# Optimization experiments

Hardware: AMD Instinct MI355X
Metric: run time of the kernel (lower is better)

## Reference

```python
import jax, jax.numpy as jnp
import numpy as np

# Dimensions
NT, NS = 1000, 2048   # timesteps, basins
NF, NG = 6, 32        # forcing channels, static attributes
NH, NR, HS = 16, 8, 256  # buckets, routing taps, hidden size
NK, NGD = 3, 9        # len(kDict)=3 (km,ki,ke), len(gDict)=9


def setup_inputs() -> dict:
    key = jax.random.key(0)
    ks = jax.random.split(key, 16)
    # Physically plausible forcings: Prcp/Evp nonnegative, T1<=T2 (min/max temp)
    Prcp = jax.random.uniform(ks[0], (NT, NS)) * 10.0
    Evp = jax.random.uniform(ks[1], (NT, NS)) * 5.0
    Tm = jax.random.normal(ks[2], (NT, NS)) * 10.0
    T1 = Tm - jax.random.uniform(ks[3], (NT, NS)) * 5.0
    T2 = Tm + jax.random.uniform(ks[4], (NT, NS)) * 5.0
    Rad = jax.random.uniform(ks[5], (NT, NS))
    Hum = jax.random.uniform(ks[6], (NT, NS))
    x = jnp.stack([Prcp, Evp, T1, T2, Rad, Hum], axis=-1)  # [nt, ns, 6]
    xc = jax.random.normal(ks[7], (NS, NG))

    def lin(k, fan_in, fan_out, s=0.05):
        k1, k2 = jax.random.split(k)
        return (jax.random.normal(k1, (fan_in, fan_out)) * s,
                jax.random.normal(k2, (fan_out,)) * s)

    W_fc, b_fc = lin(ks[8], NG, HS)
    W_r, b_r = lin(ks[9], HS, NH * (NR + 1))
    W_g, b_g = lin(ks[10], HS, NH * NGD)
    W_kin, b_kin = lin(ks[11], 4, HS)
    W_kout, b_kout = lin(ks[12], HS, NH * NK)
    return dict(x=x, xc=xc, W_fc=W_fc, b_fc=b_fc, W_r=W_r, b_r=b_r,
                W_g=W_g, b_g=b_g, W_kin=W_kin, b_kin=b_kin,
                W_kout=W_kout, b_kout=b_kout)


def _hardsigmoid(v):
    return jnp.clip(v / 6.0 + 0.5, 0.0, 1.0)


def _forward(x, xc, W_fc, b_fc, W_r, b_r, W_g, b_g, W_kin, b_kin, W_kout, b_kout):
    nt, ns, _ = x.shape
    Prcp, Evp, T1, T2 = x[..., 0], x[..., 1], x[..., 2], x[..., 3]
    f = x[..., 2:]                        # [nt, ns, 4] (T1,T2,Rad,Hum)

    # ---- getParam (eval mode: DropMask is identity) ----
    state = xc @ W_fc + b_fc              # [ns, hs]
    pK = jnp.tanh(f @ W_kin + b_kin + state) @ W_kout + b_kout  # [nt, ns, nh*3]
    hG = jnp.tanh(state)
    pG = hG @ W_g + b_g                   # [ns, nh*9]
    pR = hG @ W_r + b_r                   # [ns, nh*(nr+1)]

    # sepParam(K): km=exp, ki=relu, ke=exp  -> time-varying [nt, ns, nh]
    km = jnp.exp(pK[..., 0 * NH:1 * NH])
    ki = jax.nn.relu(pK[..., 1 * NH:2 * NH])
    ke = jnp.exp(pK[..., 2 * NH:3 * NH])

    # sepParam(G): static [ns, nh]
    g = lambda i: pG[..., i * NH:(i + 1) * NH]
    kp = jax.nn.sigmoid(g(0))
    ks_ = jax.nn.sigmoid(g(1))
    kd = jax.nn.sigmoid(g(2))
    gd = jax.nn.sigmoid(g(3))
    gl = (jax.nn.sigmoid(g(4)) * 10.0) ** 3
    qb = jax.nn.relu(g(5)) / 10.0
    ga = jax.nn.softmax(g(6), axis=-1)    # area weights over buckets
    gi = _hardsigmoid(g(7)) / 2.0
    ge = jax.nn.relu(g(8))

    # onePeakWeight: unimodal routing weights [ns, nh, nr]
    r = pR.reshape(ns, NH, NR + 1)
    s = jax.nn.softmax(r, axis=-1)
    c = jnp.cumsum(s, axis=-1)
    w = jnp.minimum(c, 1.0 - c + s)[..., :NR]
    wr = w / jnp.sum(w, axis=-1, keepdims=True)

    # divideP: snow/liquid split from min/max temperature crossing 0 C
    fl = jnp.clip(T2 / (T2 - T1 + 1e-5), 0.0, 1.0)  # liquid fraction
    Pl = (Prcp * fl)[..., None]           # [nt, ns, 1]
    Ps = (Prcp * (1.0 - fl))[..., None]
    Ev = Evp[..., None]

    # ---- bucket.step recurrence over time (the custom-scan hot loop) ----
    def step(carry, inp):
        Sf, Ss, Sg = carry                # each [ns, nh]
        Ps_t, Pl_t, Ev_t, km_t, ki_t, ke_t = inp
        # snow bucket: accumulate, melt capped by degree-day factor km
        Sf = Sf + Ps_t
        qf = jnp.minimum(Sf, km_t)
        Sf = Sf - qf
        # partition inflow: impervious/direct fraction gi
        inflow = qf + Pl_t
        qd = inflow * gi
        Ss = Ss + inflow * (1.0 - gi)
        # evapotranspiration
        E = jnp.minimum(jnp.maximum(Ss, 0.0), Ev_t * ke_t * ge)
        Ss = Ss - E
        # interflow capped by ki
        qi = jnp.minimum(ki_t, jnp.maximum(Ss, 0.0))
        Ss = Ss - qi
        # quick flow above capacity gl, slow drainage below
        qp = kp * jnp.maximum(Ss - gl, 0.0)
        qsa = ks_ * jnp.clip(Ss, 0.0, gl)
        Ss = Ss - qp - qsa
        # deep/groundwater bucket: fraction gd percolates, linear reservoir kd + baseflow qb
        Sg = Sg + qsa * gd
        qg = kd * Sg + qb
        Sg = Sg * (1.0 - kd)
        q = qp + qsa * (1.0 - gd) + qg + qd + qi
        return (Sf, Ss, Sg), q

    init = (jnp.zeros((ns, NH), x.dtype),
            jnp.zeros((ns, NH), x.dtype),
            jnp.zeros((ns, NH), x.dtype))
    _, Qp = jax.lax.scan(step, init, (Ps, Pl, Ev, km, ki, ke))  # [nt, ns, nh]

    # routing: valid temporal convolution with per-bucket unit hydrograph wr
    Tout = nt - NR + 1
    Q = jnp.zeros((Tout, ns, NH), Qp.dtype)
    for rr in range(NR):  # NR is a small fixed constant
        Q = Q + Qp[NR - 1 - rr: nt - rr] * wr[..., rr]
    yOut = jnp.sum(Q * ga, axis=-1)       # [Tout, ns]
    return yOut


def reference(x, xc, W_fc, b_fc, W_r, b_r, W_g, b_g, W_kin, b_kin, W_kout, b_kout):
    return _forward(x, xc, W_fc, b_fc, W_r, b_r, W_g, b_g, W_kin, b_kin, W_kout, b_kout)
```

## Files before the change

### kernel.cpp

```cpp
#include <hip/hip_runtime.h>
#include <hip/hip_bf16.h>

#define NT   1000
#define NS   2048
#define NH   16
#define NR   8
#define HS   256
#define TOUT 993

typedef __attribute__((ext_vector_type(8))) short short8;
typedef __attribute__((ext_vector_type(4))) float f32x4;

__device__ __forceinline__ ushort f2bf(float f) {
    union { float f; unsigned int u; } v; v.f = f;
    unsigned int u = v.u;
    return (ushort)((u + 0x7fffu + ((u >> 16) & 1u)) >> 16);
}
__device__ __forceinline__ float bf2f(ushort u) {
    union { unsigned int i; float f; } v; v.i = ((unsigned int)u) << 16; return v.f;
}
__device__ __forceinline__ unsigned int packbf2(float lo, float hi) {
    union { __hip_bfloat162 b; unsigned int u; } v;
    v.b = __float22bfloat162_rn(make_float2(lo, hi));
    return v.u;
}
__device__ __forceinline__ float sigf(float x) { return 1.f / (1.f + __expf(-x)); }
__device__ __forceinline__ float fast_tanh(float z) {
    float e = exp2f(z * 2.885390082f);
    return 1.f - 2.f * __builtin_amdgcn_rcpf(e + 1.f);
}
template<int CTRL>
__device__ __forceinline__ float dpp_add(float v) {
    int s = __builtin_amdgcn_update_dpp(0, __builtin_bit_cast(int, v), CTRL, 0xf, 0xf, true);
    return v + __builtin_bit_cast(float, s);
}
__device__ __forceinline__ void gll16(const void* g, void* l) {
    __builtin_amdgcn_global_load_lds((const __attribute__((address_space(1))) unsigned int*)g,
                                     (__attribute__((address_space(3))) unsigned int*)l, 16, 0, 0);
}
__device__ __forceinline__ void gll4(const void* g, void* l) {
    __builtin_amdgcn_global_load_lds((const __attribute__((address_space(1))) unsigned int*)g,
                                     (__attribute__((address_space(3))) unsigned int*)l, 4, 0, 0);
}


__global__ __launch_bounds__(256) void kAw(
    const float* __restrict__ W_g, const float* __restrict__ W_r,
    const float* __restrict__ W_kin, const float* __restrict__ W_kout,
    ushort* __restrict__ WAhi, ushort* __restrict__ WAlo,
    ushort* __restrict__ Wt_g, ushort* __restrict__ whlo_g)
{
    const int tid = threadIdx.x, b = blockIdx.x;
    const int idx = b * 256 + tid;
    const int j = idx & 7, lane = (idx >> 3) & 63, chunk = idx >> 9;
    const int kc = chunk & 7, ct = chunk >> 3;
    const int col = ct * 16 + (lane & 15);
    const int k = kc * 32 + (lane >> 4) * 8 + j;
    const float* W = (col < 144) ? W_g : W_r;
    const int c2 = (col < 144) ? col : col - 144;
    const float w = W[k * 144 + c2];
    const ushort hi = f2bf(w);
    WAhi[idx] = hi;
    WAlo[idx] = f2bf(w - bf2f(hi));

    if (b == 0) {
        for (int i = tid; i < 48 * 256; i += 256) {
            int c = i % 48, slot = i / 48;
            int kk2 = slot >> 5, q = (slot >> 3) & 3, jj = slot & 7;
            int h = kk2 * 32 + ((jj < 4) ? (q * 4 + jj) : (16 + q * 4 + (jj - 4)));
            Wt_g[c * 264 + slot] = f2bf(W_kout[h * 48 + c]);
        }
        const int h = tid;
#pragma unroll
        for (int f = 0; f < 4; ++f) {
            float w2 = W_kin[f * 256 + h];
            ushort hi2 = f2bf(w2);
            whlo_g[h * 8 + f] = hi2;
            whlo_g[h * 8 + 4 + f] = f2bf(w2 - bf2f(hi2));
        }
    }
}

__global__ __launch_bounds__(256) void kA1(
    const float* __restrict__ xc, const float* __restrict__ W_fc,
    const float* __restrict__ b_fc, const float* __restrict__ b_kin,
    float* __restrict__ stateK, ushort* __restrict__ hGh, ushort* __restrict__ hGl)
{
    __shared__ float xcs[32];
    const int s = blockIdx.x, tid = threadIdx.x;
    if (tid < 32) xcs[tid] = xc[s * 32 + tid];
    __syncthreads();
    float acc = b_fc[tid];
#pragma unroll 8
    for (int k = 0; k < 32; ++k) acc = fmaf(xcs[k], W_fc[k * 256 + tid], acc);
    stateK[s * 256 + tid] = acc + b_kin[tid];
    float hg = tanhf(acc);
    ushort hi = f2bf(hg);
    hGh[s * 256 + tid] = hi;
    hGl[s * 256 + tid] = f2bf(hg - bf2f(hi));
}

__global__ __launch_bounds__(256) void kA2(
    const ushort* __restrict__ hGh, const ushort* __restrict__ hGl,
    const ushort* __restrict__ WAhi, const ushort* __restrict__ WAlo,
    const float* __restrict__ b_g, const float* __restrict__ b_r,
    float* __restrict__ params)
{
    __shared__ ushort hGhS[16][264];
    __shared__ ushort hGlS[16][264];
    __shared__ float  pGRS[16][292];
    const int tid = threadIdx.x;
    const int s0 = blockIdx.x * 16;

    for (int i = tid; i < 512; i += 256) {
        int site = i >> 5, off = (i & 31) * 8;
        *(uint4*)&hGhS[site][off] = *(const uint4*)&hGh[(s0 + site) * 256 + off];
        *(uint4*)&hGlS[site][off] = *(const uint4*)&hGl[(s0 + site) * 256 + off];
    }
    __syncthreads();

    const int wv = tid >> 6, lane = tid & 63;
    const int n = lane & 15, q = lane >> 4;
    for (int ct = wv; ct < 18; ct += 4) {
        f32x4 acc = (f32x4){0.f, 0.f, 0.f, 0.f};
#pragma unroll
        for (int kc = 0; kc < 8; ++kc) {
            const int fidx = ((ct * 8 + kc) * 64 + lane) * 8;
            short8 awh = *(const short8*)(WAhi + fidx);
            short8 awl = *(const short8*)(WAlo + fidx);
            short8 bhh = *(const short8*)&hGhS[n][kc * 32 + q * 8];
            short8 bhl = *(const short8*)&hGlS[n][kc * 32 + q * 8];
            acc = __builtin_amdgcn_mfma_f32_16x16x32_bf16(awh, bhh, acc, 0, 0, 0);
            acc = __builtin_amdgcn_mfma_f32_16x16x32_bf16(awl, bhh, acc, 0, 0, 0);
            acc = __builtin_amdgcn_mfma_f32_16x16x32_bf16(awh, bhl, acc, 0, 0, 0);
        }
#pragma unroll
        for (int r = 0; r < 4; ++r) pGRS[n][ct * 16 + q * 4 + r] = acc[r];
    }
    __syncthreads();

    const int sl = tid >> 4, h = tid & 15;
    const int s = s0 + sl;
    float g0 = pGRS[sl][0 * 16 + h] + b_g[0 * 16 + h];
    float g1 = pGRS[sl][1 * 16 + h] + b_g[1 * 16 + h];
    float g2 = pGRS[sl][2 * 16 + h] + b_g[2 * 16 + h];
    float g3 = pGRS[sl][3 * 16 + h] + b_g[3 * 16 + h];
    float g4 = pGRS[sl][4 * 16 + h] + b_g[4 * 16 + h];
    float g5 = pGRS[sl][5 * 16 + h] + b_g[5 * 16 + h];
    float g6 = pGRS[sl][6 * 16 + h] + b_g[6 * 16 + h];
    float g7 = pGRS[sl][7 * 16 + h] + b_g[7 * 16 + h];
    float g8 = pGRS[sl][8 * 16 + h] + b_g[8 * 16 + h];
    float kp = sigf(g0), ksg = sigf(g1), kd = sigf(g2), gd = sigf(g3);
    float t4 = sigf(g4) * 10.f; float gl = t4 * t4 * t4;
    float qb = fmaxf(g5, 0.f) * 0.1f;
    float gi = fminf(fmaxf(g7 * (1.f / 6.f) + 0.5f, 0.f), 1.f) * 0.5f;
    float ge = fmaxf(g8, 0.f);
    float m = g6;
    for (int o = 1; o < 16; o <<= 1) m = fmaxf(m, __shfl_xor(m, o));
    float e = __expf(g6 - m), esum = e;
    for (int o = 1; o < 16; o <<= 1) esum += __shfl_xor(esum, o);
    float ga = e / esum;
    float r9[9], rm = -1e30f;
#pragma unroll
    for (int i = 0; i < 9; ++i) {
        r9[i] = pGRS[sl][144 + h * 9 + i] + b_r[h * 9 + i];
        rm = fmaxf(rm, r9[i]);
    }
    float er[9], es = 0.f;
#pragma unroll
    for (int i = 0; i < 9; ++i) { er[i] = __expf(r9[i] - rm); es += er[i]; }
    float inv_es = 1.f / es, c = 0.f, wsum = 0.f, w[8];
#pragma unroll
    for (int i = 0; i < 8; ++i) {
        float si = er[i] * inv_es; c += si;
        float wi = fminf(c, 1.f - c + si);
        w[i] = wi; wsum += wi;
    }
    const int base = s * 16 + h;
    params[0 * 32768 + base] = kp;       params[1 * 32768 + base] = ksg;
    params[2 * 32768 + base] = kd;       params[3 * 32768 + base] = gd;
    params[4 * 32768 + base] = gl;       params[5 * 32768 + base] = qb;
    params[6 * 32768 + base] = gi;       params[7 * 32768 + base] = 1.f - gi;
    params[8 * 32768 + base] = 1.f - kd; params[9 * 32768 + base] = 1.f - gd;
    params[10 * 32768 + base] = ge;
    float sc = ga / wsum;
#pragma unroll
    for (int i = 0; i < 8; ++i) params[(11 + i) * 32768 + base] = w[i] * sc;
}

__global__ __launch_bounds__(256, 3) void kB(
    const float* __restrict__ x,
    const float* __restrict__ stateK, const float* __restrict__ b_kout,
    const ushort* __restrict__ Wt_g, const ushort* __restrict__ whlo_g,
    const float* __restrict__ params,
    unsigned int* __restrict__ kmki, ushort* __restrict__ kevA,
    float2* __restrict__ pspl)
{
    __shared__ ushort Wt[48 * 264];
    __shared__ float  stS[16 * 260];
    __shared__ ushort whloS[2048];
    __shared__ float  geS[256];
    __shared__ float  evS[4][5][16];
    const int tid = threadIdx.x;
    const int st = blockIdx.x & 127;
    const int tg = blockIdx.x >> 7;
    const int s0 = st << 4;

    for (int i = tid; i < 3168; i += 256)
        ((uint2*)Wt)[i] = ((const uint2*)Wt_g)[i];
#pragma unroll
    for (int i = tid; i < 1024; i += 256) {
        int row = i >> 6, c = (i & 63) << 2;
        *(float4*)(stS + row * 260 + c) = *(const float4*)(stateK + (s0 + row) * 256 + c);
    }
    *(float4*)(whloS + tid * 8) = ((const float4*)whlo_g)[tid];
    geS[tid] = params[10 * 32768 + s0 * 16 + tid];
    __syncthreads();

    const int wv = tid >> 6, lane = tid & 63;
    const int mi = lane & 15, quad = lane >> 4;
    const int site = s0 + mi;
    const int t0 = tg * 20 + wv * 5;

    float xf[5][4];
#pragma unroll
    for (int ti = 0; ti < 5; ++ti) {
        const int t = t0 + ti;
        const int xb = (t * 2048 + site) * 6;
        float2 u23 = *(const float2*)(x + xb + 2);
        float2 u45 = *(const float2*)(x + xb + 4);
        xf[ti][0] = u23.x; xf[ti][1] = u23.y; xf[ti][2] = u45.x; xf[ti][3] = u45.y;
        if (lane < 16) {
            float2 u01 = *(const float2*)(x + xb);
            float fl = fminf(fmaxf(u23.y * __builtin_amdgcn_rcpf(u23.y - u23.x + 1e-5f), 0.f), 1.f);
            const int sg = st * 4 + (mi >> 2), sl = mi & 3;
            pspl[(sg * 1000 + t) * 4 + sl] = make_float2(u01.x * (1.f - fl), u01.x * fl);
            evS[wv][ti][mi] = u01.y;
        }
    }

    unsigned int bfr[5][4];
#pragma unroll
    for (int ti = 0; ti < 5; ++ti) {
        const float x0 = xf[ti][0], x1 = xf[ti][1], x2 = xf[ti][2], x3 = xf[ti][3];
        unsigned int h01 = packbf2(x0, x1), h23 = packbf2(x2, x3);
        float l0 = x0 - bf2f((ushort)(h01 & 0xffffu));
        float l1 = x1 - bf2f((ushort)(h01 >> 16));
        float l2 = x2 - bf2f((ushort)(h23 & 0xffffu));
        float l3 = x3 - bf2f((ushort)(h23 >> 16));
        unsigned int l01 = packbf2(l0, l1), l23 = packbf2(l2, l3);
        bfr[ti][0] = (quad == 0) ? h01 : (quad == 1 ? l01 : 0u);
        bfr[ti][1] = (quad == 0) ? h23 : (quad == 1 ? l23 : 0u);
        bfr[ti][2] = (quad == 0) ? h01 : 0u;
        bfr[ti][3] = (quad == 0) ? h23 : 0u;
    }

    const float*  stp = stS + mi * 260;
    const ushort* Wt0 = Wt + mi * 264 + quad * 8;
    const int q4 = quad * 4;

    f32x4 acc[5][3];
#pragma unroll
    for (int ti = 0; ti < 5; ++ti)
#pragma unroll
        for (int j = 0; j < 3; ++j) acc[ti][j] = (f32x4){0.f, 0.f, 0.f, 0.f};

#pragma unroll 1
    for (int kk = 0; kk < 8; ++kk) {
        const int ko = kk * 32;
        union { short8 s; unsigned int u[4]; } W0, W1, A0, A1;
        W0.s = *(const short8*)(whloS + (ko + mi) * 8);
        W1.s = *(const short8*)(whloS + (ko + 16 + mi) * 8);
        A0.u[0] = (quad <= 1) ? W0.u[0] : 0u;
        A0.u[1] = (quad <= 1) ? W0.u[1] : 0u;
        A0.u[2] = (quad == 0) ? W0.u[2] : 0u;
        A0.u[3] = (quad == 0) ? W0.u[3] : 0u;
        A1.u[0] = (quad <= 1) ? W1.u[0] : 0u;
        A1.u[1] = (quad <= 1) ? W1.u[1] : 0u;
        A1.u[2] = (quad == 0) ? W1.u[2] : 0u;
        A1.u[3] = (quad == 0) ? W1.u[3] : 0u;
        f32x4 c0 = *(const f32x4*)(stp + ko + q4);
        f32x4 c1 = *(const f32x4*)(stp + ko + 16 + q4);
        short8 b0 = *(const short8*)(Wt0 + ko);
        short8 b1 = *(const short8*)(Wt0 + 16 * 264 + ko);
        short8 b2 = *(const short8*)(Wt0 + 32 * 264 + ko);
#pragma unroll
        for (int ti = 0; ti < 5; ++ti) {
            union { short8 s; unsigned int u[4]; } B;
            B.u[0] = bfr[ti][0]; B.u[1] = bfr[ti][1];
            B.u[2] = bfr[ti][2]; B.u[3] = bfr[ti][3];
            f32x4 z0 = __builtin_amdgcn_mfma_f32_16x16x32_bf16(A0.s, B.s, c0, 0, 0, 0);
            f32x4 z1 = __builtin_amdgcn_mfma_f32_16x16x32_bf16(A1.s, B.s, c1, 0, 0, 0);
            union { short8 s; unsigned int u[4]; } a;
            a.u[0] = packbf2(fast_tanh(z0[0]), fast_tanh(z0[1]));
            a.u[1] = packbf2(fast_tanh(z0[2]), fast_tanh(z0[3]));
            a.u[2] = packbf2(fast_tanh(z1[0]), fast_tanh(z1[1]));
            a.u[3] = packbf2(fast_tanh(z1[2]), fast_tanh(z1[3]));
            acc[ti][0] = __builtin_amdgcn_mfma_f32_16x16x32_bf16(a.s, b0, acc[ti][0], 0, 0, 0);
            acc[ti][1] = __builtin_amdgcn_mfma_f32_16x16x32_bf16(a.s, b1, acc[ti][1], 0, 0, 0);
            acc[ti][2] = __builtin_amdgcn_mfma_f32_16x16x32_bf16(a.s, b2, acc[ti][2], 0, 0, 0);
        }
    }

    const float bo0 = b_kout[mi], bo1 = b_kout[16 + mi], bo2 = b_kout[32 + mi];
#pragma unroll
    for (int ti = 0; ti < 5; ++ti) {
        const int t = t0 + ti;
#pragma unroll
        for (int reg = 0; reg < 4; ++reg) {
            const int sl = quad * 4 + reg;
            float km = __expf(acc[ti][0][reg] + bo0);
            float ki = fmaxf(acc[ti][1][reg] + bo1, 0.f);
            float ke = __expf(acc[ti][2][reg] + bo2);
            float kev = ke * evS[wv][ti][sl] * geS[sl * 16 + mi];
            const int idx = ((s0 + sl) * 1000 + t) * 16 + mi;
            kmki[idx] = (unsigned int)f2bf(km) | ((unsigned int)f2bf(ki) << 16);
            kevA[idx] = f2bf(kev);
        }
    }
}

#define KM_STRIDE 4160
#define KE_BASE   16640
#define KE_STRIDE 2080
#define PS_BASE   24960
#define BUF_SZ    27008
__global__ __launch_bounds__(64, 1) void kC(
    const unsigned int* __restrict__ kmki, const ushort* __restrict__ kevA,
    const float2* __restrict__ pspl,
    const float* __restrict__ params, float* __restrict__ yOut)
{
    __shared__ char lds[2 * BUF_SZ];
    const int tid = threadIdx.x;
    const int sg = blockIdx.x;
    const int sl = tid >> 4;
    const int s = sg * 4 + sl;
    const int h = tid & 15;
    const int gid = s * 16 + h;

    const float kp  = params[0 * 32768 + gid];
    const float ks_ = params[1 * 32768 + gid];
    const float kd  = params[2 * 32768 + gid];
    const float gd  = params[3 * 32768 + gid];
    const float gl  = params[4 * 32768 + gid];
    const float qbv = params[5 * 32768 + gid];
    const float gi  = params[6 * 32768 + gid];
    const float gi1 = params[7 * 32768 + gid];
    const float kd1 = params[8 * 32768 + gid];
    const float gd1 = params[9 * 32768 + gid];
    float wrga[8];
#pragma unroll
    for (int i = 0; i < 8; ++i) wrga[i] = params[(11 + i) * 32768 + gid];

    float Sf = 0.f, Ss = 0.f, Sg = 0.f;
    float qcur[8], qp1[8], qp2[8];
#pragma unroll
    for (int i = 0; i < 8; ++i) { qcur[i] = 0.f; qp1[i] = 0.f; qp2[i] = 0.f; }

    const char* kmG = (const char*)kmki;
    const char* keG = (const char*)kevA;
    const char* psG = (const char*)pspl;

#define STAGE(c, TAIL) do {                                                     \
        char* L = lds + ((c) & 1) * BUF_SZ;                                     \
        _Pragma("unroll")                                                       \
        for (int q = 0; q < 4; ++q) {                                           \
            const char* gk = kmG + ((size_t)(sg * 4 + q) * 1000 + (c) * 64) * 64; \
            const char* ge = keG + ((size_t)(sg * 4 + q) * 1000 + (c) * 64) * 32; \
            char* lk = L + q * KM_STRIDE;                                       \
            char* le = L + KE_BASE + q * KE_STRIDE;                             \
            if (!(TAIL)) {                                                      \
                _Pragma("unroll")                                               \
                for (int k = 0; k < 4; ++k) gll16(gk + k * 1024 + tid * 16, lk + k * 1024); \
                _Pragma("unroll")                                               \
                for (int k = 0; k < 2; ++k) gll16(ge + k * 1024 + tid * 16, le + k * 1024); \
            } else {                                                            \
                _Pragma("unroll")                                               \
                for (int k = 0; k < 2; ++k) gll16(gk + k * 1024 + tid * 16, lk + k * 1024); \
                _Pragma("unroll")                                               \
                for (int k = 0; k < 2; ++k) gll4(gk + 2048 + k * 256 + tid * 4, lk + 2048 + k * 256); \
                gll16(ge + tid * 16, le);                                       \
                gll4(ge + 1024 + tid * 4, le + 1024);                           \
            }                                                                   \
        }                                                                       \
        const char* gp = psG + ((size_t)sg * 1000 + (c) * 64) * 32;             \
        char* lp = L + PS_BASE;                                                 \
        if (!(TAIL)) { gll16(gp + tid * 16, lp); gll16(gp + 1024 + tid * 16, lp + 1024); } \
        else         { gll16(gp + tid * 16, lp); gll4(gp + 1024 + tid * 4, lp + 1024); }   \
    } while (0)

#define SCANB(c, sb) do {                                                       \
        const char* L = lds + ((c) & 1) * BUF_SZ;                               \
        const char* lk = L + sl * KM_STRIDE + h * 4 + (sb) * 512;               \
        const char* le = L + KE_BASE + sl * KE_STRIDE + h * 2 + (sb) * 256;     \
        const char* lp = L + PS_BASE + sl * 8 + (sb) * 256;                     \
        unsigned int a[8]; ushort e[8]; float2 p[8];                            \
        _Pragma("unroll")                                                       \
        for (int i = 0; i < 8; ++i) {                                           \
            a[i] = *(const unsigned int*)(lk + i * 64);                         \
            e[i] = *(const ushort*)(le + i * 32);                               \
            p[i] = *(const float2*)(lp + i * 32);                               \
        }                                                                       \
        _Pragma("unroll")                                                       \
        for (int i = 0; i < 8; ++i) {                                           \
            float km = __builtin_bit_cast(float, a[i] << 16);                   \
            float ki = __builtin_bit_cast(float, a[i] & 0xffff0000u);           \
            float kev = __builtin_bit_cast(float, ((unsigned int)e[i]) << 16);  \
            float ps = p[i].x, pl = p[i].y;                                     \
            Sf += ps;                                                           \
            float qf = fminf(Sf, km); Sf -= qf;                                 \
            float inflow = qf + pl;                                             \
            float qd = inflow * gi;                                             \
            Ss = fmaf(inflow, gi1, Ss);                                         \
            float E = fminf(Ss, kev); Ss -= E;                                  \
            float qi = fminf(ki, Ss); Ss -= qi;                                 \
            float qp = kp * fmaxf(Ss - gl, 0.f);                                \
            float qsa = ks_ * fminf(Ss, gl);                                    \
            Ss -= qp + qsa;                                                     \
            Sg = fmaf(qsa, gd, Sg);                                             \
            float qg = fmaf(kd, Sg, qbv);                                       \
            Sg *= kd1;                                                          \
            qcur[i] = fmaf(qsa, gd1, qp) + qg + qd + qi;                        \
        }                                                                       \
    } while (0)

#define CONV_STORE(m) do {                                                      \
        float z[8];                                                             \
        _Pragma("unroll")                                                       \
        for (int i = 0; i < 8; ++i) {                                           \
            float za = wrga[6] * ((i >= 6) ? qp1[i - 6] : qp2[i + 2]);          \
            za = fmaf(wrga[4], (i >= 4) ? qp1[i - 4] : qp2[i + 4], za);         \
            za = fmaf(wrga[2], (i >= 2) ? qp1[i - 2] : qp2[i + 6], za);         \
            za = fmaf(wrga[0], qp1[i], za);                                     \
            float zb = wrga[7] * ((i >= 7) ? qp1[i - 7] : qp2[i + 1]);          \
            zb = fmaf(wrga[5], (i >= 5) ? qp1[i - 5] : qp2[i + 3], zb);         \
            zb = fmaf(wrga[3], (i >= 3) ? qp1[i - 3] : qp2[i + 5], zb);         \
            zb = fmaf(wrga[1], (i >= 1) ? qp1[i - 1] : qp2[i + 7], zb);         \
            z[i] = za + zb;                                                     \
        }                                                                       \
        _Pragma("unroll")                                                       \
        for (int i = 0; i < 8; ++i) z[i] = dpp_add<0xB1>(z[i]);                 \
        _Pragma("unroll")                                                       \
        for (int i = 0; i < 8; ++i) z[i] = dpp_add<0x4E>(z[i]);                 \
        _Pragma("unroll")                                                       \
        for (int i = 0; i < 8; ++i) z[i] = dpp_add<0x141>(z[i]);                \
        _Pragma("unroll")                                                       \
        for (int i = 0; i < 8; ++i) z[i] = dpp_add<0x140>(z[i]);                \
        if (h == 0) {                                                           \
            _Pragma("unroll")                                                   \
            for (int i = 0; i < 8; ++i) {                                       \
                const int t = (m) * 8 + i;                                      \
                if (t >= 7) yOut[(t - 7) * 2048 + s] = z[i];                    \
            }                                                                   \
        }                                                                       \
    } while (0)

    STAGE(0, false);
    int g = 0;
#pragma unroll 1
    for (int c = 0; c < 16; ++c) {
        if (c < 15) {
            if (c + 1 == 15) STAGE(15, true);
            else             STAGE(c + 1, false);
            asm volatile("s_waitcnt vmcnt(26)" ::: "memory");
        } else {
            asm volatile("s_waitcnt vmcnt(0)" ::: "memory");
        }
        const int NSB = (c == 15) ? 5 : 8;
#pragma unroll 1
        for (int sb = 0; sb < NSB; ++sb, ++g) {
            SCANB(c, sb);
            CONV_STORE(g - 1);
#pragma unroll
            for (int i = 0; i < 8; ++i) { qp2[i] = qp1[i]; qp1[i] = qcur[i]; }
        }
        asm volatile("" ::: "memory");
    }
    CONV_STORE(124);
#undef STAGE
#undef SCANB
#undef CONV_STORE
}

extern "C" void kernel_launch(void* const* d_in, const int* in_sizes, int n_in,
                              void* d_out, int out_size, void* d_ws, size_t ws_size,
                              hipStream_t stream) {
    const float* x      = (const float*)d_in[0];
    const float* xc     = (const float*)d_in[1];
    const float* W_fc   = (const float*)d_in[2];
    const float* b_fc   = (const float*)d_in[3];
    const float* W_r    = (const float*)d_in[4];
    const float* b_r    = (const float*)d_in[5];
    const float* W_g    = (const float*)d_in[6];
    const float* b_g    = (const float*)d_in[7];
    const float* W_kin  = (const float*)d_in[8];
    const float* b_kin  = (const float*)d_in[9];
    const float* W_kout = (const float*)d_in[10];
    const float* b_kout = (const float*)d_in[11];
    float* yOut = (float*)d_out;

    char* ws = (char*)d_ws;
    float*  stateK = (float*)(ws + 0);
    float*  params = (float*)(ws + (2 << 20));
    ushort* Wt_g   = (ushort*)(ws + (6 << 20));
    ushort* whlo_g = (ushort*)(ws + (6 << 20) + (64 << 10));
    char*   p      = ws + (6 << 20) + (128 << 10);
    float2* pspl   = (float2*)p;
    unsigned int* kmki = (unsigned int*)(p + 16384000);
    ushort* kevA   = (ushort*)(p + 16384000 + 131072000);

    ushort* hGh  = (ushort*)kmki;
    ushort* hGl  = hGh + 2048 * 256;
    ushort* WAhi = hGl + 2048 * 256;
    ushort* WAlo = WAhi + 73728;

    hipLaunchKernelGGL(kAw, dim3(288), dim3(256), 0, stream,
                       W_g, W_r, W_kin, W_kout, WAhi, WAlo, Wt_g, whlo_g);
    hipLaunchKernelGGL(kA1, dim3(2048), dim3(256), 0, stream,
                       xc, W_fc, b_fc, b_kin, stateK, hGh, hGl);
    hipLaunchKernelGGL(kA2, dim3(128), dim3(256), 0, stream,
                       hGh, hGl, WAhi, WAlo, b_g, b_r, params);
    hipLaunchKernelGGL(kB, dim3(128 * 50), dim3(256), 0, stream,
                       x, stateK, b_kout, Wt_g, whlo_g, params, kmki, kevA, pspl);
    hipLaunchKernelGGL(kC, dim3(512), dim3(64), 0, stream,
                       kmki, kevA, pspl, params, yOut);
}
```

Baseline: 479.1 us.

## Deepen kC prefetch to four smaller stages, fuse weight prep into kA1

```diff
diff --git a/kernel.cpp b/kernel.cpp
--- a/kernel.cpp
+++ b/kernel.cpp
@@ -44,47 +44,14 @@
 }
 
 
-__global__ __launch_bounds__(256) void kAw(
-    const float* __restrict__ W_g, const float* __restrict__ W_r,
-    const float* __restrict__ W_kin, const float* __restrict__ W_kout,
-    ushort* __restrict__ WAhi, ushort* __restrict__ WAlo,
-    ushort* __restrict__ Wt_g, ushort* __restrict__ whlo_g)
-{
-    const int tid = threadIdx.x, b = blockIdx.x;
-    const int idx = b * 256 + tid;
-    const int j = idx & 7, lane = (idx >> 3) & 63, chunk = idx >> 9;
-    const int kc = chunk & 7, ct = chunk >> 3;
-    const int col = ct * 16 + (lane & 15);
-    const int k = kc * 32 + (lane >> 4) * 8 + j;
-    const float* W = (col < 144) ? W_g : W_r;
-    const int c2 = (col < 144) ? col : col - 144;
-    const float w = W[k * 144 + c2];
-    const ushort hi = f2bf(w);
-    WAhi[idx] = hi;
-    WAlo[idx] = f2bf(w - bf2f(hi));
-
-    if (b == 0) {
-        for (int i = tid; i < 48 * 256; i += 256) {
-            int c = i % 48, slot = i / 48;
-            int kk2 = slot >> 5, q = (slot >> 3) & 3, jj = slot & 7;
-            int h = kk2 * 32 + ((jj < 4) ? (q * 4 + jj) : (16 + q * 4 + (jj - 4)));
-            Wt_g[c * 264 + slot] = f2bf(W_kout[h * 48 + c]);
-        }
-        const int h = tid;
-#pragma unroll
-        for (int f = 0; f < 4; ++f) {
-            float w2 = W_kin[f * 256 + h];
-            ushort hi2 = f2bf(w2);
-            whlo_g[h * 8 + f] = hi2;
-            whlo_g[h * 8 + 4 + f] = f2bf(w2 - bf2f(hi2));
-        }
-    }
-}
-
 __global__ __launch_bounds__(256) void kA1(
     const float* __restrict__ xc, const float* __restrict__ W_fc,
     const float* __restrict__ b_fc, const float* __restrict__ b_kin,
-    float* __restrict__ stateK, ushort* __restrict__ hGh, ushort* __restrict__ hGl)
+    const float* __restrict__ W_g, const float* __restrict__ W_r,
+    const float* __restrict__ W_kin, const float* __restrict__ W_kout,
+    float* __restrict__ stateK, ushort* __restrict__ hGh, ushort* __restrict__ hGl,
+    ushort* __restrict__ WAhi, ushort* __restrict__ WAlo,
+    ushort* __restrict__ Wt_g, ushort* __restrict__ whlo_g)
 {
     __shared__ float xcs[32];
     const int s = blockIdx.x, tid = threadIdx.x;
@@ -98,6 +65,36 @@
     ushort hi = f2bf(hg);
     hGh[s * 256 + tid] = hi;
     hGl[s * 256 + tid] = f2bf(hg - bf2f(hi));
+
+    if (s < 288) {
+        const int idx = s * 256 + tid;
+        const int j = idx & 7, lane = (idx >> 3) & 63, chunk = idx >> 9;
+        const int kc = chunk & 7, ct = chunk >> 3;
+        const int col = ct * 16 + (lane & 15);
+        const int k = kc * 32 + (lane >> 4) * 8 + j;
+        const float* W = (col < 144) ? W_g : W_r;
+        const int c2 = (col < 144) ? col : col - 144;
+        const float w = W[k * 144 + c2];
+        const ushort whi = f2bf(w);
+        WAhi[idx] = whi;
+        WAlo[idx] = f2bf(w - bf2f(whi));
+    }
+    if (s == 0) {
+        for (int i = tid; i < 48 * 256; i += 256) {
+            int c = i % 48, slot = i / 48;
+            int kk2 = slot >> 5, q = (slot >> 3) & 3, jj = slot & 7;
+            int h = kk2 * 32 + ((jj < 4) ? (q * 4 + jj) : (16 + q * 4 + (jj - 4)));
+            Wt_g[c * 264 + slot] = f2bf(W_kout[h * 48 + c]);
+        }
+        const int h = tid;
+#pragma unroll
+        for (int f = 0; f < 4; ++f) {
+            float w2 = W_kin[f * 256 + h];
+            ushort hi2 = f2bf(w2);
+            whlo_g[h * 8 + f] = hi2;
+            whlo_g[h * 8 + 4 + f] = f2bf(w2 - bf2f(hi2));
+        }
+    }
 }
 
 __global__ __launch_bounds__(256) void kA2(
@@ -314,23 +311,23 @@
             float ke = __expf(acc[ti][2][reg] + bo2);
             float kev = ke * evS[wv][ti][sl] * geS[sl * 16 + mi];
             const int idx = ((s0 + sl) * 1000 + t) * 16 + mi;
-            kmki[idx] = (unsigned int)f2bf(km) | ((unsigned int)f2bf(ki) << 16);
-            kevA[idx] = f2bf(kev);
-        }
-    }
-}
-
-#define KM_STRIDE 4160
-#define KE_BASE   16640
-#define KE_STRIDE 2080
-#define PS_BASE   24960
-#define BUF_SZ    27008
+            kmki[idx] = packbf2(km, ki);
+            kevA[idx] = (ushort)(packbf2(kev, kev) & 0xffffu);
+        }
+    }
+}
+
+#define KM_STRIDE 2112
+#define KE_BASE   8448
+#define KE_STRIDE 1056
+#define PS_BASE   12672
+#define BUF_SZ    13696
 __global__ __launch_bounds__(64, 1) void kC(
     const unsigned int* __restrict__ kmki, const ushort* __restrict__ kevA,
     const float2* __restrict__ pspl,
     const float* __restrict__ params, float* __restrict__ yOut)
 {
-    __shared__ char lds[2 * BUF_SZ];
+    __shared__ char lds[4 * BUF_SZ];
     const int tid = threadIdx.x;
     const int sg = blockIdx.x;
     const int sl = tid >> 4;
@@ -362,35 +359,31 @@
     const char* psG = (const char*)pspl;
 
 #define STAGE(c, TAIL) do {                                                     \
-        char* L = lds + ((c) & 1) * BUF_SZ;                                     \
+        char* L = lds + ((c) & 3) * BUF_SZ;                                     \
         _Pragma("unroll")                                                       \
         for (int q = 0; q < 4; ++q) {                                           \
-            const char* gk = kmG + ((size_t)(sg * 4 + q) * 1000 + (c) * 64) * 64; \
-            const char* ge = keG + ((size_t)(sg * 4 + q) * 1000 + (c) * 64) * 32; \
+            const char* gk = kmG + ((size_t)(sg * 4 + q) * 1000 + (c) * 32) * 64; \
+            const char* ge = keG + ((size_t)(sg * 4 + q) * 1000 + (c) * 32) * 32; \
             char* lk = L + q * KM_STRIDE;                                       \
             char* le = L + KE_BASE + q * KE_STRIDE;                             \
             if (!(TAIL)) {                                                      \
-                _Pragma("unroll")                                               \
-                for (int k = 0; k < 4; ++k) gll16(gk + k * 1024 + tid * 16, lk + k * 1024); \
-                _Pragma("unroll")                                               \
-                for (int k = 0; k < 2; ++k) gll16(ge + k * 1024 + tid * 16, le + k * 1024); \
+                gll16(gk + tid * 16, lk);                                       \
+                gll16(gk + 1024 + tid * 16, lk + 1024);                         \
+                gll16(ge + tid * 16, le);                                       \
             } else {                                                            \
-                _Pragma("unroll")                                               \
-                for (int k = 0; k < 2; ++k) gll16(gk + k * 1024 + tid * 16, lk + k * 1024); \
-                _Pragma("unroll")                                               \
-                for (int k = 0; k < 2; ++k) gll4(gk + 2048 + k * 256 + tid * 4, lk + 2048 + k * 256); \
-                gll16(ge + tid * 16, le);                                       \
-                gll4(ge + 1024 + tid * 4, le + 1024);                           \
+                gll4(gk + tid * 4, lk);                                         \
+                gll4(gk + 256 + tid * 4, lk + 256);                             \
+                gll4(ge + tid * 4, le);                                         \
             }                                                                   \
         }                                                                       \
-        const char* gp = psG + ((size_t)sg * 1000 + (c) * 64) * 32;             \
+        const char* gp = psG + ((size_t)sg * 1000 + (c) * 32) * 32;             \
         char* lp = L + PS_BASE;                                                 \
-        if (!(TAIL)) { gll16(gp + tid * 16, lp); gll16(gp + 1024 + tid * 16, lp + 1024); } \
-        else         { gll16(gp + tid * 16, lp); gll4(gp + 1024 + tid * 4, lp + 1024); }   \
+        if (!(TAIL)) gll16(gp + tid * 16, lp);                                  \
+        else         gll4(gp + tid * 4, lp);                                    \
     } while (0)
 
 #define SCANB(c, sb) do {                                                       \
-        const char* L = lds + ((c) & 1) * BUF_SZ;                               \
+        const char* L = lds + ((c) & 3) * BUF_SZ;                               \
         const char* lk = L + sl * KM_STRIDE + h * 4 + (sb) * 512;               \
         const char* le = L + KE_BASE + sl * KE_STRIDE + h * 2 + (sb) * 256;     \
         const char* lp = L + PS_BASE + sl * 8 + (sb) * 256;                     \
@@ -456,17 +449,18 @@
     } while (0)
 
     STAGE(0, false);
+    STAGE(1, false);
+    STAGE(2, false);
     int g = 0;
 #pragma unroll 1
-    for (int c = 0; c < 16; ++c) {
-        if (c < 15) {
-            if (c + 1 == 15) STAGE(15, true);
-            else             STAGE(c + 1, false);
-            asm volatile("s_waitcnt vmcnt(26)" ::: "memory");
-        } else {
-            asm volatile("s_waitcnt vmcnt(0)" ::: "memory");
-        }
-        const int NSB = (c == 15) ? 5 : 8;
+    for (int c = 0; c < 32; ++c) {
+        if (c + 3 <= 30)      STAGE(c + 3, false);
+        else if (c + 3 == 31) STAGE(31, true);
+        if (c <= 28)      asm volatile("s_waitcnt vmcnt(39)" ::: "memory");
+        else if (c == 29) asm volatile("s_waitcnt vmcnt(26)" ::: "memory");
+        else if (c == 30) asm volatile("s_waitcnt vmcnt(13)" ::: "memory");
+        else              asm volatile("s_waitcnt vmcnt(0)"  ::: "memory");
+        const int NSB = (c == 31) ? 1 : 4;
 #pragma unroll 1
         for (int sb = 0; sb < NSB; ++sb, ++g) {
             SCANB(c, sb);
@@ -514,10 +508,9 @@
     ushort* WAhi = hGl + 2048 * 256;
     ushort* WAlo = WAhi + 73728;
 
-    hipLaunchKernelGGL(kAw, dim3(288), dim3(256), 0, stream,
-                       W_g, W_r, W_kin, W_kout, WAhi, WAlo, Wt_g, whlo_g);
     hipLaunchKernelGGL(kA1, dim3(2048), dim3(256), 0, stream,
-                       xc, W_fc, b_fc, b_kin, stateK, hGh, hGl);
+                       xc, W_fc, b_fc, b_kin, W_g, W_r, W_kin, W_kout,
+                       stateK, hGh, hGl, WAhi, WAlo, Wt_g, whlo_g);
     hipLaunchKernelGGL(kA2, dim3(128), dim3(256), 0, stream,
                        hGh, hGl, WAhi, WAlo, b_g, b_r, params);
     hipLaunchKernelGGL(kB, dim3(128 * 50), dim3(256), 0, stream,
```

Measured after the change: 479.3 us. About the same (+0.1%).
